# Optimization experiments

Measured on AMD Instinct MI355X. Metric: run time of the kernel, lower is better.

Reference implementation:

```python
import jax, jax.numpy as jnp
import numpy as np

HIDDEN = 1024
HEADS = 16
HEAD_DIM = HIDDEN // HEADS


def setup_inputs() -> dict:
    key = jax.random.key(0)
    ks = jax.random.split(key, 9)
    s = 1.0 / np.sqrt(HIDDEN)
    inp = {
        "x": jax.random.normal(ks[0], (2, 2048, HIDDEN), dtype=jnp.float32),
        "Wq": jax.random.uniform(ks[1], (HIDDEN, HIDDEN), jnp.float32, -s, s),
        "bq": jax.random.uniform(ks[2], (HIDDEN,), jnp.float32, -s, s),
        "Wk": jax.random.uniform(ks[3], (HIDDEN, HIDDEN), jnp.float32, -s, s),
        "bk": jax.random.uniform(ks[4], (HIDDEN,), jnp.float32, -s, s),
        "Wv": jax.random.uniform(ks[5], (HIDDEN, HIDDEN), jnp.float32, -s, s),
        "bv": jax.random.uniform(ks[6], (HIDDEN,), jnp.float32, -s, s),
        "Wo": jax.random.uniform(ks[7], (HIDDEN, HIDDEN), jnp.float32, -s, s),
        "bo": jax.random.uniform(ks[8], (HIDDEN,), jnp.float32, -s, s),
    }
    return inp


def reference(x, Wq, bq, Wk, bk, Wv, bv, Wo, bo):
    B, S, _ = x.shape
    # QKV projections; reshape to [B, H, S, D]
    def heads(t):
        return t.reshape(B, S, HEADS, HEAD_DIM).transpose(0, 2, 1, 3)
    q = heads(x @ Wq + bq)
    k = heads(x @ Wk + bk)
    v = heads(x @ Wv + bv)
    scale = 1.0 / np.sqrt(HEAD_DIM)
    scores = jnp.einsum('bhqd,bhkd->bhqk', q, k) * scale  # [B,H,S,S]
    attn = jax.nn.softmax(scores, axis=-1)
    out = jnp.einsum('bhqk,bhkd->bhqd', attn, v)  # [B,H,S,D]
    out = out.transpose(0, 2, 1, 3).reshape(B, S, HIDDEN)
    return out @ Wo + bo
```

## Files before the change

kernel.cpp:

```cpp
#include <hip/hip_runtime.h>
#include <math.h>


namespace {

constexpr int kHID = 1024;
constexpr int kNH  = 16;
constexpr int kHD  = 64;
constexpr int kSEQ = 2048;

constexpr float kQScale = 0.125f * 1.4426950408889634f;

typedef unsigned short ushortT;
typedef __attribute__((ext_vector_type(8))) short   bf16x8;
typedef __attribute__((ext_vector_type(4))) float   f32x4;
typedef __attribute__((ext_vector_type(4))) unsigned short u16x4;

#define MFMA(a, b, c) __builtin_amdgcn_mfma_f32_16x16x32_bf16((a), (b), (c), 0, 0, 0)

typedef const __attribute__((address_space(1))) void GVoid;
typedef __attribute__((address_space(3))) void SVoid;

__device__ __forceinline__ void gload_lds16(const ushortT* g, ushortT* l) {
    __builtin_amdgcn_global_load_lds((GVoid*)g, (SVoid*)l, 16, 0, 0);
}

__device__ __forceinline__ ushortT f2bf(float f) {
    unsigned u = __builtin_bit_cast(unsigned, f);
    u += 0x7fffu + ((u >> 16) & 1u);
    return (ushortT)(u >> 16);
}

__device__ __forceinline__ unsigned cvt_pk_bf16(float a, float b) {
    unsigned r;
    asm("v_cvt_pk_bf16_f32 %0, %1, %2" : "=v"(r) : "v"(a), "v"(b));
    return r;
}

__device__ __forceinline__ float4 ld4f(const float* p) { return *reinterpret_cast<const float4*>(p); }

__global__ __launch_bounds__(256) void cvtx_kernel(const float* __restrict__ x,
                                                   ushortT* __restrict__ xb) {
    const size_t i = ((size_t)blockIdx.x * 256 + threadIdx.x) * 4;
    const float4 f = ld4f(&x[i]);
    u16x4 o = { f2bf(f.x), f2bf(f.y), f2bf(f.z), f2bf(f.w) };
    *reinterpret_cast<u16x4*>(&xb[i]) = o;
}

__global__ __launch_bounds__(256) void transw_kernel(
    const float* __restrict__ W0, const float* __restrict__ W1,
    const float* __restrict__ W2, const float* __restrict__ W3,
    ushortT* __restrict__ WtAll) {
    __shared__ ushortT T[64 * 72];
    const float* W = (blockIdx.z == 0) ? W0 : (blockIdx.z == 1) ? W1 : (blockIdx.z == 2) ? W2 : W3;
    ushortT* Wt = WtAll + (size_t)blockIdx.z * kHID * kHID;
    const int kb = blockIdx.y * 64, nb = blockIdx.x * 64;
    const int tid = threadIdx.x;
    {
        const int kr = tid >> 2, nc = (tid & 3) * 16;
        #pragma unroll
        for (int i = 0; i < 16; i += 4) {
            const float4 f = ld4f(&W[(size_t)(kb + kr) * kHID + nb + nc + i]);
            T[kr * 72 + nc + i + 0] = f2bf(f.x);
            T[kr * 72 + nc + i + 1] = f2bf(f.y);
            T[kr * 72 + nc + i + 2] = f2bf(f.z);
            T[kr * 72 + nc + i + 3] = f2bf(f.w);
        }
    }
    __syncthreads();
    {
        const int nr = tid >> 2, kc = (tid & 3) * 16;
        ushortT tmp[16];
        #pragma unroll
        for (int i = 0; i < 16; ++i) tmp[i] = T[(kc + i) * 72 + nr];
        *reinterpret_cast<bf16x8*>(&Wt[(size_t)(nb + nr) * kHID + kb + kc]) =
            *reinterpret_cast<bf16x8*>(&tmp[0]);
        *reinterpret_cast<bf16x8*>(&Wt[(size_t)(nb + nr) * kHID + kb + kc + 8]) =
            *reinterpret_cast<bf16x8*>(&tmp[8]);
    }
}

template <typename Epi>
__device__ __forceinline__ void gemm128_body(
    const ushortT* __restrict__ A, const ushortT* __restrict__ Bt,
    int rowBase, int colBase, ushortT* As, ushortT* Bs, Epi&& epi) {
    const int tid = threadIdx.x, wid = tid >> 6, lane = tid & 63;
    const int hi = lane >> 4, lo = lane & 15;
    const int wr = wid >> 1, wc = wid & 1;
    const int r8 = lane >> 3, jc = lane & 7;

    const f32x4 z4 = {0.f, 0.f, 0.f, 0.f};
    f32x4 acc[4][4];
    #pragma unroll
    for (int mi = 0; mi < 4; ++mi)
        #pragma unroll
        for (int ni = 0; ni < 4; ++ni) acc[mi][ni] = z4;

    auto STAGE = [&](int buf, int k0) {
        #pragma unroll
        for (int i = 0; i < 4; ++i) {
            const int chunk = wid * 4 + i;
            const int row = chunk * 8 + r8;
            const int c8 = 8 * (jc ^ r8);
            gload_lds16(&A [(size_t)(rowBase + row) * kHID + k0 + c8], &As[buf * 8192 + chunk * 512]);
            gload_lds16(&Bt[(size_t)(colBase + row) * kHID + k0 + c8], &Bs[buf * 8192 + chunk * 512]);
        }
    };

    STAGE(0, 0);
    __syncthreads();
    int cur = 0;

    for (int k0 = 0; k0 < kHID; k0 += 64) {
        if (k0 + 64 < kHID) STAGE(cur ^ 1, k0 + 64);

        __builtin_amdgcn_s_setprio(1);
        #pragma unroll
        for (int ks = 0; ks < 2; ++ks) {
            bf16x8 af[4], bfr[4];
            #pragma unroll
            for (int mi = 0; mi < 4; ++mi) {
                const int row = 64 * wr + 16 * mi + lo;
                af[mi] = *reinterpret_cast<const bf16x8*>(
                    &As[cur * 8192 + row * 64 + 8 * ((4 * ks + hi) ^ (row & 7))]);
            }
            #pragma unroll
            for (int ni = 0; ni < 4; ++ni) {
                const int row = 64 * wc + 16 * ni + lo;
                bfr[ni] = *reinterpret_cast<const bf16x8*>(
                    &Bs[cur * 8192 + row * 64 + 8 * ((4 * ks + hi) ^ (row & 7))]);
            }
            #pragma unroll
            for (int mi = 0; mi < 4; ++mi)
                #pragma unroll
                for (int ni = 0; ni < 4; ++ni)
                    acc[mi][ni] = MFMA(af[mi], bfr[ni], acc[mi][ni]);
        }
        __builtin_amdgcn_s_setprio(0);

        __syncthreads();
        cur ^= 1;
    }

    epi(acc, wr, wc, hi, lo);
}

__global__ __launch_bounds__(256, 2) void qkv_mfma_gemm(
    const ushortT* __restrict__ A, const ushortT* __restrict__ WtAll,
    const float* __restrict__ bq, const float* __restrict__ bk, const float* __restrict__ bv,
    ushortT* __restrict__ qkvb) {
    __shared__ ushortT As[2 * 8192];
    __shared__ ushortT Bs[2 * 8192];

    const int z = blockIdx.z;
    const ushortT* Bt = WtAll + (size_t)z * kHID * kHID;
    const float* bias = (z == 0) ? bq : (z == 1) ? bk : bv;
    ushortT* out = qkvb + (size_t)z * 2 * kNH * kSEQ * kHD;
    const float scale = (z == 0) ? kQScale : 1.0f;
    const int rowBase = blockIdx.y * 128, colBase = blockIdx.x * 128;

    gemm128_body(A, Bt, rowBase, colBase, As, Bs,
        [&](f32x4 (&acc)[4][4], int wr, int wc, int hi, int lo) {
            #pragma unroll
            for (int ni = 0; ni < 4; ++ni) {
                const int col = colBase + 64 * wc + 16 * ni + lo;
                const float bcol = bias[col];
                const int h = col >> 6, d = col & 63;
                #pragma unroll
                for (int mi = 0; mi < 4; ++mi)
                    #pragma unroll
                    for (int r = 0; r < 4; ++r) {
                        const int m = rowBase + 64 * wr + 16 * mi + 4 * hi + r;
                        const int b = m >> 11, s = m & (kSEQ - 1);
                        const ushortT val = f2bf((acc[mi][ni][r] + bcol) * scale);
                        if (z == 2)
                            out[(((size_t)b * kNH + h) * kHD + d) * kSEQ + s] = val;
                        else
                            out[(((size_t)b * kNH + h) * kSEQ + s) * kHD + d] = val;
                    }
            }
        });
}

__global__ __launch_bounds__(256, 2) void out_mfma_gemm(
    const ushortT* __restrict__ A, const ushortT* __restrict__ Bt,
    const float* __restrict__ bias, float* __restrict__ out) {
    __shared__ ushortT As[2 * 8192];
    __shared__ ushortT Bs[2 * 8192];

    const int rowBase = blockIdx.y * 128, colBase = blockIdx.x * 128;

    gemm128_body(A, Bt, rowBase, colBase, As, Bs,
        [&](f32x4 (&acc)[4][4], int wr, int wc, int hi, int lo) {
            #pragma unroll
            for (int ni = 0; ni < 4; ++ni) {
                const int col = colBase + 64 * wc + 16 * ni + lo;
                const float bcol = bias[col];
                #pragma unroll
                for (int mi = 0; mi < 4; ++mi)
                    #pragma unroll
                    for (int r = 0; r < 4; ++r) {
                        const int m = rowBase + 64 * wr + 16 * mi + 4 * hi + r;
                        out[(size_t)m * kHID + col] = acc[mi][ni][r] + bcol;
                    }
            }
        });
}

__global__ __launch_bounds__(256, 4) void flash_mfma_kernel(
    const ushortT* __restrict__ Qb, const ushortT* __restrict__ Kb,
    const ushortT* __restrict__ Vtg, ushortT* __restrict__ Ob) {
    __shared__ ushortT Ks[2][64 * 64];
    __shared__ ushortT Vs[2][64 * 64];

    const int tid = threadIdx.x, wid = tid >> 6, lane = tid & 63;
    const int hi = lane >> 4, lo = lane & 15;
    const int q0 = blockIdx.x * 64;
    const size_t headBase = ((size_t)blockIdx.z * kNH + blockIdx.y) * (size_t)(kSEQ * kHD);
    const ushortT* Kg = Kb + headBase;
    const ushortT* Vg = Vtg + headBase;

    bf16x8 qf[2];
    #pragma unroll
    for (int c = 0; c < 2; ++c)
        qf[c] = *reinterpret_cast<const bf16x8*>(
            &Qb[headBase + (size_t)(q0 + 16 * wid + lo) * kHD + 32 * c + 8 * hi]);

    const short one = (short)0x3F80;
    const bf16x8 ones = {one, one, one, one, one, one, one, one};

    const f32x4 z4 = {0.f, 0.f, 0.f, 0.f};
    f32x4 acc[4] = {z4, z4, z4, z4};
    f32x4 accL = z4;

    const int r8 = lane >> 3, jc = lane & 7;

    const int kap0 = 8 * (lo >> 2) + (lo & 3);
    const int sk = (lo & 3) | (((lo >> 2) & 1) << 2);
    const int kx0 = (8 * hi) ^ (sk << 3);
    const int kx1 = (32 + 8 * hi) ^ (sk << 3);
    const int sv = (lo & 3) | (((lo >> 3) & 1) << 2);

    auto STAGE = [&](int buf, int kv0) {
        #pragma unroll
        for (int i = 0; i < 2; ++i) {
            const int rowBase = (i * 4 + wid) * 8;
            const int row = rowBase + r8;
            const int s8 = (r8 & 3) | ((wid & 1) << 2);
            gload_lds16(&Kg[(size_t)(kv0 + row) * kHD + 8 * (jc ^ s8)], &Ks[buf][rowBase * 64]);
            gload_lds16(&Vg[(size_t)row * kSEQ + kv0 + 8 * (jc ^ s8)], &Vs[buf][rowBase * 64]);
        }
    };

    STAGE(0, 0);
    __syncthreads();
    int cur = 0;

    for (int t = 0; t < kSEQ / 64; ++t) {
        if (t + 1 < kSEQ / 64) STAGE(cur ^ 1, (t + 1) * 64);

        f32x4 sc[4];
        __builtin_amdgcn_s_setprio(1);
        #pragma unroll
        for (int f = 0; f < 4; ++f) {
            const int kap = kap0 + 4 * (f & 1) + 32 * (f >> 1);
            const bf16x8 kf0 = *reinterpret_cast<const bf16x8*>(&Ks[cur][kap * 64 + kx0]);
            const bf16x8 kf1 = *reinterpret_cast<const bf16x8*>(&Ks[cur][kap * 64 + kx1]);
            sc[f] = MFMA(kf1, qf[1], MFMA(kf0, qf[0], z4));
        }
        __builtin_amdgcn_s_setprio(0);

        float p[4][4];
        #pragma unroll
        for (int f = 0; f < 4; ++f)
            #pragma unroll
            for (int r = 0; r < 4; ++r) p[f][r] = exp2f(sc[f][r]);

        union U { unsigned u[4]; bf16x8 v; };
        U pa0, pa1;
        pa0.u[0] = cvt_pk_bf16(p[0][0], p[0][1]);
        pa0.u[1] = cvt_pk_bf16(p[0][2], p[0][3]);
        pa0.u[2] = cvt_pk_bf16(p[1][0], p[1][1]);
        pa0.u[3] = cvt_pk_bf16(p[1][2], p[1][3]);
        pa1.u[0] = cvt_pk_bf16(p[2][0], p[2][1]);
        pa1.u[1] = cvt_pk_bf16(p[2][2], p[2][3]);
        pa1.u[2] = cvt_pk_bf16(p[3][0], p[3][1]);
        pa1.u[3] = cvt_pk_bf16(p[3][2], p[3][3]);

        __builtin_amdgcn_s_setprio(1);
        accL = MFMA(pa0.v, ones, accL);
        accL = MFMA(pa1.v, ones, accL);
        #pragma unroll
        for (int n = 0; n < 4; ++n) {
            const int vrow = 16 * n + lo;
            const bf16x8 vf0 = *reinterpret_cast<const bf16x8*>(
                &Vs[cur][vrow * 64 + ((8 * hi) ^ (sv << 3))]);
            const bf16x8 vf1 = *reinterpret_cast<const bf16x8*>(
                &Vs[cur][vrow * 64 + ((32 + 8 * hi) ^ (sv << 3))]);
            acc[n] = MFMA(pa0.v, vf0, acc[n]);
            acc[n] = MFMA(pa1.v, vf1, acc[n]);
        }
        __builtin_amdgcn_s_setprio(0);

        __syncthreads();
        cur ^= 1;
    }

    #pragma unroll
    for (int r = 0; r < 4; ++r) {
        const float inv = 1.0f / accL[r];
        const int s = q0 + 16 * wid + 4 * hi + r;
        const size_t base = ((size_t)blockIdx.z * kSEQ + s) * kHID + (size_t)blockIdx.y * kHD;
        #pragma unroll
        for (int n = 0; n < 4; ++n)
            Ob[base + 16 * n + lo] = f2bf(acc[n][r] * inv);
    }
}

}

extern "C" void kernel_launch(void* const* d_in, const int* in_sizes, int n_in,
                              void* d_out, int out_size, void* d_ws, size_t ws_size,
                              hipStream_t stream) {
    (void)in_sizes; (void)n_in; (void)out_size;
    const float* x  = (const float*)d_in[0];
    const float* Wq = (const float*)d_in[1];
    const float* bq = (const float*)d_in[2];
    const float* Wk = (const float*)d_in[3];
    const float* bk = (const float*)d_in[4];
    const float* Wv = (const float*)d_in[5];
    const float* bv = (const float*)d_in[6];
    const float* Wo = (const float*)d_in[7];
    const float* bo = (const float*)d_in[8];

    constexpr size_t kXE = (size_t)2 * kSEQ * kHID;
    constexpr size_t kWE = (size_t)kHID * kHID;
    const size_t needed = (kXE + 4 * kWE + 3 * kXE + kXE) * sizeof(ushortT);
    if (ws_size < needed) return;

    ushortT* xb    = (ushortT*)d_ws;
    ushortT* WtAll = xb + kXE;
    ushortT* qkvb  = WtAll + 4 * kWE;
    ushortT* attnb = qkvb + 3 * kXE;

    const ushortT* qb  = qkvb;
    const ushortT* kb  = qkvb + kXE;
    const ushortT* vtb = qkvb + 2 * kXE;

    cvtx_kernel<<<dim3((unsigned)(kXE / (256 * 4))), 256, 0, stream>>>(x, xb);
    transw_kernel<<<dim3(16, 16, 4), 256, 0, stream>>>(Wq, Wk, Wv, Wo, WtAll);

    qkv_mfma_gemm<<<dim3(8, 32, 3), 256, 0, stream>>>(xb, WtAll, bq, bk, bv, qkvb);

    flash_mfma_kernel<<<dim3(kSEQ / 64, kNH, 2), 256, 0, stream>>>(qb, kb, vtb, attnb);

    out_mfma_gemm<<<dim3(8, 32), 256, 0, stream>>>(attnb, WtAll + 3 * kWE, bo, (float*)d_out);
}
```

Measured before the change: 139.9 us.

## Have each flash wave process two 16-row query tiles with 128-thread blocks

The attention kernel now uses 2 waves per block, and each wave handles 32 query rows as two 16-row sub-tiles. The K and V fragments read from LDS are reused across both sub-tiles, which halves LDS reads per MFMA. The grid is also reordered so the head index is the fastest-varying block dimension, which changes which blocks run together and share K/V in cache. The cost is more accumulator registers per wave and fewer waves per block to hide latency.

```diff
diff --git a/kernel.cpp b/kernel.cpp
--- a/kernel.cpp
+++ b/kernel.cpp
@@ -207,7 +207,7 @@
         });
 }
 
-__global__ __launch_bounds__(256, 4) void flash_mfma_kernel(
+__global__ __launch_bounds__(128) void flash_mfma_kernel(
     const ushortT* __restrict__ Qb, const ushortT* __restrict__ Kb,
     const ushortT* __restrict__ Vtg, ushortT* __restrict__ Ob) {
     __shared__ ushortT Ks[2][64 * 64];
@@ -215,23 +215,27 @@
 
     const int tid = threadIdx.x, wid = tid >> 6, lane = tid & 63;
     const int hi = lane >> 4, lo = lane & 15;
-    const int q0 = blockIdx.x * 64;
-    const size_t headBase = ((size_t)blockIdx.z * kNH + blockIdx.y) * (size_t)(kSEQ * kHD);
+    const int h = blockIdx.x;
+    const int q0 = blockIdx.y * 64 + 32 * wid;
+    const size_t headBase = ((size_t)blockIdx.z * kNH + h) * (size_t)(kSEQ * kHD);
     const ushortT* Kg = Kb + headBase;
     const ushortT* Vg = Vtg + headBase;
 
-    bf16x8 qf[2];
+    bf16x8 qf[2][2];
     #pragma unroll
-    for (int c = 0; c < 2; ++c)
-        qf[c] = *reinterpret_cast<const bf16x8*>(
-            &Qb[headBase + (size_t)(q0 + 16 * wid + lo) * kHD + 32 * c + 8 * hi]);
+    for (int s = 0; s < 2; ++s)
+        #pragma unroll
+        for (int c = 0; c < 2; ++c)
+            qf[s][c] = *reinterpret_cast<const bf16x8*>(
+                &Qb[headBase + (size_t)(q0 + 16 * s + lo) * kHD + 32 * c + 8 * hi]);
 
     const short one = (short)0x3F80;
     const bf16x8 ones = {one, one, one, one, one, one, one, one};
 
     const f32x4 z4 = {0.f, 0.f, 0.f, 0.f};
-    f32x4 acc[4] = {z4, z4, z4, z4};
-    f32x4 accL = z4;
+    f32x4 accA[4] = {z4, z4, z4, z4};
+    f32x4 accB[4] = {z4, z4, z4, z4};
+    f32x4 accLA = z4, accLB = z4;
 
     const int r8 = lane >> 3, jc = lane & 7;
 
@@ -243,8 +247,8 @@
 
     auto STAGE = [&](int buf, int kv0) {
         #pragma unroll
-        for (int i = 0; i < 2; ++i) {
-            const int rowBase = (i * 4 + wid) * 8;
+        for (int i = 0; i < 4; ++i) {
+            const int rowBase = (i * 2 + wid) * 8;
             const int row = rowBase + r8;
             const int s8 = (r8 & 3) | ((wid & 1) << 2);
             gload_lds16(&Kg[(size_t)(kv0 + row) * kHD + 8 * (jc ^ s8)], &Ks[buf][rowBase * 64]);
@@ -259,37 +263,56 @@
     for (int t = 0; t < kSEQ / 64; ++t) {
         if (t + 1 < kSEQ / 64) STAGE(cur ^ 1, (t + 1) * 64);
 
-        f32x4 sc[4];
+        f32x4 scA[4], scB[4];
         __builtin_amdgcn_s_setprio(1);
         #pragma unroll
         for (int f = 0; f < 4; ++f) {
             const int kap = kap0 + 4 * (f & 1) + 32 * (f >> 1);
             const bf16x8 kf0 = *reinterpret_cast<const bf16x8*>(&Ks[cur][kap * 64 + kx0]);
             const bf16x8 kf1 = *reinterpret_cast<const bf16x8*>(&Ks[cur][kap * 64 + kx1]);
-            sc[f] = MFMA(kf1, qf[1], MFMA(kf0, qf[0], z4));
+            scA[f] = MFMA(kf1, qf[0][1], MFMA(kf0, qf[0][0], z4));
+            scB[f] = MFMA(kf1, qf[1][1], MFMA(kf0, qf[1][0], z4));
         }
         __builtin_amdgcn_s_setprio(0);
 
-        float p[4][4];
-        #pragma unroll
-        for (int f = 0; f < 4; ++f)
-            #pragma unroll
-            for (int r = 0; r < 4; ++r) p[f][r] = exp2f(sc[f][r]);
-
         union U { unsigned u[4]; bf16x8 v; };
-        U pa0, pa1;
-        pa0.u[0] = cvt_pk_bf16(p[0][0], p[0][1]);
-        pa0.u[1] = cvt_pk_bf16(p[0][2], p[0][3]);
-        pa0.u[2] = cvt_pk_bf16(p[1][0], p[1][1]);
-        pa0.u[3] = cvt_pk_bf16(p[1][2], p[1][3]);
-        pa1.u[0] = cvt_pk_bf16(p[2][0], p[2][1]);
-        pa1.u[1] = cvt_pk_bf16(p[2][2], p[2][3]);
-        pa1.u[2] = cvt_pk_bf16(p[3][0], p[3][1]);
-        pa1.u[3] = cvt_pk_bf16(p[3][2], p[3][3]);
+        U paA0, paA1, paB0, paB1;
+        {
+            float p[4][4];
+            #pragma unroll
+            for (int f = 0; f < 4; ++f)
+                #pragma unroll
+                for (int r = 0; r < 4; ++r) p[f][r] = exp2f(scA[f][r]);
+            paA0.u[0] = cvt_pk_bf16(p[0][0], p[0][1]);
+            paA0.u[1] = cvt_pk_bf16(p[0][2], p[0][3]);
+            paA0.u[2] = cvt_pk_bf16(p[1][0], p[1][1]);
+            paA0.u[3] = cvt_pk_bf16(p[1][2], p[1][3]);
+            paA1.u[0] = cvt_pk_bf16(p[2][0], p[2][1]);
+            paA1.u[1] = cvt_pk_bf16(p[2][2], p[2][3]);
+            paA1.u[2] = cvt_pk_bf16(p[3][0], p[3][1]);
+            paA1.u[3] = cvt_pk_bf16(p[3][2], p[3][3]);
+        }
+        {
+            float p[4][4];
+            #pragma unroll
+            for (int f = 0; f < 4; ++f)
+                #pragma unroll
+                for (int r = 0; r < 4; ++r) p[f][r] = exp2f(scB[f][r]);
+            paB0.u[0] = cvt_pk_bf16(p[0][0], p[0][1]);
+            paB0.u[1] = cvt_pk_bf16(p[0][2], p[0][3]);
+            paB0.u[2] = cvt_pk_bf16(p[1][0], p[1][1]);
+            paB0.u[3] = cvt_pk_bf16(p[1][2], p[1][3]);
+            paB1.u[0] = cvt_pk_bf16(p[2][0], p[2][1]);
+            paB1.u[1] = cvt_pk_bf16(p[2][2], p[2][3]);
+            paB1.u[2] = cvt_pk_bf16(p[3][0], p[3][1]);
+            paB1.u[3] = cvt_pk_bf16(p[3][2], p[3][3]);
+        }
 
         __builtin_amdgcn_s_setprio(1);
-        accL = MFMA(pa0.v, ones, accL);
-        accL = MFMA(pa1.v, ones, accL);
+        accLA = MFMA(paA0.v, ones, accLA);
+        accLA = MFMA(paA1.v, ones, accLA);
+        accLB = MFMA(paB0.v, ones, accLB);
+        accLB = MFMA(paB1.v, ones, accLB);
         #pragma unroll
         for (int n = 0; n < 4; ++n) {
             const int vrow = 16 * n + lo;
@@ -297,8 +320,10 @@
                 &Vs[cur][vrow * 64 + ((8 * hi) ^ (sv << 3))]);
             const bf16x8 vf1 = *reinterpret_cast<const bf16x8*>(
                 &Vs[cur][vrow * 64 + ((32 + 8 * hi) ^ (sv << 3))]);
-            acc[n] = MFMA(pa0.v, vf0, acc[n]);
-            acc[n] = MFMA(pa1.v, vf1, acc[n]);
+            accA[n] = MFMA(paA0.v, vf0, accA[n]);
+            accA[n] = MFMA(paA1.v, vf1, accA[n]);
+            accB[n] = MFMA(paB0.v, vf0, accB[n]);
+            accB[n] = MFMA(paB1.v, vf1, accB[n]);
         }
         __builtin_amdgcn_s_setprio(0);
 
@@ -307,13 +332,18 @@
     }
 
     #pragma unroll
-    for (int r = 0; r < 4; ++r) {
-        const float inv = 1.0f / accL[r];
-        const int s = q0 + 16 * wid + 4 * hi + r;
-        const size_t base = ((size_t)blockIdx.z * kSEQ + s) * kHID + (size_t)blockIdx.y * kHD;
-        #pragma unroll
-        for (int n = 0; n < 4; ++n)
-            Ob[base + 16 * n + lo] = f2bf(acc[n][r] * inv);
+    for (int s = 0; s < 2; ++s) {
+        const f32x4* acc = (s == 0) ? accA : accB;
+        const f32x4& accL = (s == 0) ? accLA : accLB;
+        #pragma unroll
+        for (int r = 0; r < 4; ++r) {
+            const float inv = 1.0f / accL[r];
+            const int srow = q0 + 16 * s + 4 * hi + r;
+            const size_t base = ((size_t)blockIdx.z * kSEQ + srow) * kHID + (size_t)h * kHD;
+            #pragma unroll
+            for (int n = 0; n < 4; ++n)
+                Ob[base + 16 * n + lo] = f2bf(acc[n][r] * inv);
+        }
     }
 }
 
@@ -352,7 +382,7 @@
 
     qkv_mfma_gemm<<<dim3(8, 32, 3), 256, 0, stream>>>(xb, WtAll, bq, bk, bv, qkvb);
 
-    flash_mfma_kernel<<<dim3(kSEQ / 64, kNH, 2), 256, 0, stream>>>(qb, kb, vtb, attnb);
+    flash_mfma_kernel<<<dim3(kNH, kSEQ / 64, 2), 128, 0, stream>>>(qb, kb, vtb, attnb);
 
     out_mfma_gemm<<<dim3(8, 32), 256, 0, stream>>>(attnb, WtAll + 3 * kWE, bo, (float*)d_out);
 }
```

Result: slower. 164.2 us (+17.4%).
